# Kernel tuning notes

Hardware: AMD Instinct MI355X
Metric: run time of the kernel (lower is better)

Reference implementation:

```python
import jax, jax.numpy as jnp
import numpy as np

N_NODES = 200000
N_EDGES = 600000
IN_DIM = 130   # hidden_dim + 2
HID = 128
BN_EPS = 1e-5


def setup_inputs() -> dict:
    key = jax.random.key(0)
    ks = jax.random.split(key, 12)
    s = 0.05
    inp = {
        'x': jax.random.normal(ks[0], (N_NODES, IN_DIM), dtype=jnp.float32),
        'edge_index': jax.random.randint(ks[1], (2, N_EDGES), 0, N_NODES, dtype=jnp.int32),
        # SAGEConv 1: lin_l (aggregated neighbors, with bias), lin_r (root, no bias)
        'W1_l': jax.random.normal(ks[2], (IN_DIM, HID), dtype=jnp.float32) * s,
        'b1_l': jnp.zeros((HID,), dtype=jnp.float32),
        'W1_r': jax.random.normal(ks[3], (IN_DIM, HID), dtype=jnp.float32) * s,
        # BatchNorm1d(128) params + running stats (eval mode)
        'g1': jnp.ones((HID,), dtype=jnp.float32),
        'be1': jnp.zeros((HID,), dtype=jnp.float32),
        'rm1': jax.random.normal(ks[4], (HID,), dtype=jnp.float32) * 0.01,
        'rv1': jnp.ones((HID,), dtype=jnp.float32),
        # SAGEConv 2
        'W2_l': jax.random.normal(ks[5], (HID, HID), dtype=jnp.float32) * s,
        'b2_l': jnp.zeros((HID,), dtype=jnp.float32),
        'W2_r': jax.random.normal(ks[6], (HID, HID), dtype=jnp.float32) * s,
        'g2': jnp.ones((HID,), dtype=jnp.float32),
        'be2': jnp.zeros((HID,), dtype=jnp.float32),
        'rm2': jax.random.normal(ks[7], (HID,), dtype=jnp.float32) * 0.01,
        'rv2': jnp.ones((HID,), dtype=jnp.float32),
    }
    return inp


def _sage_mean(x, src, dst, W_l, b_l, W_r, n_nodes):
    # PyG SAGEConv (mean aggr): out = lin_l(mean_{j in N(i)} x_j) + lin_r(x_i)
    msg = x[src]                                                 # [E, F] gather
    agg = jax.ops.segment_sum(msg, dst, num_segments=n_nodes)    # [N, F]
    deg = jax.ops.segment_sum(jnp.ones((src.shape[0], 1), x.dtype), dst,
                              num_segments=n_nodes)              # [N, 1]
    mean = agg / jnp.maximum(deg, 1.0)
    return mean @ W_l + b_l + x @ W_r


def _bn_eval(x, g, b, rm, rv):
    return (x - rm) * (g * jax.lax.rsqrt(rv + BN_EPS)) + b


def reference(x, edge_index, W1_l, b1_l, W1_r, g1, be1, rm1, rv1,
              W2_l, b2_l, W2_r, g2, be2, rm2, rv2):
    src, dst = edge_index[0], edge_index[1]
    n = x.shape[0]
    h = _sage_mean(x, src, dst, W1_l, b1_l, W1_r, n)
    h = jax.nn.relu(_bn_eval(h, g1, be1, rm1, rv1))
    # dropout is identity in eval mode
    h = _sage_mean(h, src, dst, W2_l, b2_l, W2_r, n)
    h = jax.nn.relu(_bn_eval(h, g2, be2, rm2, rv2))
    return h
```

## Files before the change

### kernel.cpp

```cpp
#include <hip/hip_runtime.h>
#include <hip/hip_bf16.h>

typedef short v8s __attribute__((ext_vector_type(8)));
typedef float v4f __attribute__((ext_vector_type(4)));
typedef unsigned short v4us __attribute__((ext_vector_type(4)));

__device__ __forceinline__ unsigned short f2bf(float x) {
  union { float f; unsigned int u; } c; c.f = x;
  unsigned int u = c.u;
  return (unsigned short)((u + 0x7fffu + ((u >> 16) & 1u)) >> 16);
}
__device__ __forceinline__ float bflo(unsigned int u) {
  union { unsigned int u; float f; } c; c.u = u << 16; return c.f;
}
__device__ __forceinline__ float bfhi(unsigned int u) {
  union { unsigned int u; float f; } c; c.u = u & 0xffff0000u; return c.f;
}
__device__ __forceinline__ ushort2 pk(float2 v) {
  union { __hip_bfloat162 b; ushort2 u; } c;
  c.b = __float22bfloat162_rn(v);
  return c.u;
}
__device__ __forceinline__ v4us pk4(v4f v) {
  const ushort2 lo = pk(make_float2(v[0], v[1]));
  const ushort2 hi = pk(make_float2(v[2], v[3]));
  v4us r; r[0] = lo.x; r[1] = lo.y; r[2] = hi.x; r[3] = hi.y;
  return r;
}

__device__ __forceinline__ void pack2_dev(const float* __restrict__ Wl,
                                          const float* __restrict__ Wr,
                                          unsigned short* __restrict__ wpk,
                                          int K, int tot, int i) {
  if (i >= tot) return;
  const int kk = i & 31, n = (i >> 5) & 255, kc = i >> 13;
  const int k = kc * 32 + kk;
  float v = 0.f;
  if (k < K) v = (n < 128) ? Wl[k * 128 + n] : Wr[k * 128 + (n - 128)];
  wpk[i] = f2bf(v);
}

__global__ void setup_k(const float* __restrict__ g1, const float* __restrict__ be1,
                        const float* __restrict__ rm1, const float* __restrict__ rv1,
                        const float* __restrict__ b1,
                        const float* __restrict__ g2, const float* __restrict__ be2,
                        const float* __restrict__ rm2, const float* __restrict__ rv2,
                        const float* __restrict__ b2,
                        const float* __restrict__ W1l, const float* __restrict__ W1r,
                        const float* __restrict__ W2l, const float* __restrict__ W2r,
                        float* __restrict__ s1, float* __restrict__ t1,
                        float* __restrict__ s2, float* __restrict__ t2,
                        unsigned short* __restrict__ wp1, unsigned short* __restrict__ wp2,
                        unsigned short* __restrict__ bufA, int* __restrict__ degi,
                        int N, int NZB) {
  const int b = blockIdx.x, tid = threadIdx.x;
  if (b < NZB) {
    const int i = b * 256 + tid;
    if (i < N) degi[i] = 0;
    return;
  }
  int r = b - NZB;
  if (r < 160) { pack2_dev(W1l, W1r, wp1, 130, 5 * 8192, r * 256 + tid); return; }
  r -= 160;
  if (r < 128) { pack2_dev(W2l, W2r, wp2, 128, 4 * 8192, r * 256 + tid); return; }
  if (tid < 128) {
    float sv = g1[tid] * rsqrtf(rv1[tid] + 1e-5f);
    s1[tid] = sv; t1[tid] = (b1[tid] - rm1[tid]) * sv + be1[tid];
    float sw = g2[tid] * rsqrtf(rv2[tid] + 1e-5f);
    s2[tid] = sw; t2[tid] = (b2[tid] - rm2[tid]) * sw + be2[tid];
  }
  if (tid < 64) ((unsigned int*)(bufA + (long)N * 128))[tid] = 0u;
}

__global__ __launch_bounds__(256) void scan1_k(const int* __restrict__ degi,
                                               int* __restrict__ rowptr,
                                               int* __restrict__ bsum, int N) {
  __shared__ int sd[256];
  const int t = threadIdx.x;
  const int base = blockIdx.x * 1024 + t * 4;
  int v[4];
#pragma unroll
  for (int j = 0; j < 4; ++j) v[j] = (base + j < N) ? degi[base + j] : 0;
  const int tot = v[0] + v[1] + v[2] + v[3];
  sd[t] = tot;
  __syncthreads();
  for (int off = 1; off < 256; off <<= 1) {
    int o = (t >= off) ? sd[t - off] : 0;
    __syncthreads();
    sd[t] += o;
    __syncthreads();
  }
  int e = sd[t] - tot;
#pragma unroll
  for (int j = 0; j < 4; ++j) {
    if (base + j < N) rowptr[base + j] = e;
    e += v[j];
  }
  if (t == 255) bsum[blockIdx.x] = sd[255];
}
__global__ __launch_bounds__(256) void scan3_k(int* __restrict__ rowptr,
                                               int* __restrict__ cursor,
                                               const int* __restrict__ bsum,
                                               int N, int E) {
  __shared__ int sd[256];
  const int t = threadIdx.x;
  const int chunk = blockIdx.x >> 2;
  sd[t] = (t < chunk) ? bsum[t] : 0;
  __syncthreads();
  for (int off = 128; off >= 1; off >>= 1) {
    if (t < off) sd[t] += sd[t + off];
    __syncthreads();
  }
  const int S = sd[0];
  const int i = blockIdx.x * 256 + t;
  if (i < N) {
    const int v = rowptr[i] + S;
    rowptr[i] = v;
    cursor[i] = v;
  } else if (i == N) {
    rowptr[N] = E;
  }
}
__global__ void fill_k(const int* __restrict__ src, const int* __restrict__ dst,
                       int* __restrict__ cursor, int* __restrict__ nbr, int E) {
  int i = blockIdx.x * 256 + threadIdx.x;
  if (i < E) {
    int p = atomicAdd(&cursor[dst[i]], 1);
    nbr[p] = src[i];
  }
}

__global__ __launch_bounds__(256) void gemmc_k(const float* __restrict__ Asrc,
                                               const unsigned short* __restrict__ wpk,
                                               unsigned short* __restrict__ Ol,
                                               unsigned short* __restrict__ Or,
                                               const int* __restrict__ dst,
                                               int* __restrict__ degi,
                                               int N, int E, int ngb) {
  constexpr int KC = 5;
  constexpr int KP = KC * 32;
  constexpr int LDA = KP + 8;
  __shared__ __align__(16) unsigned short a_s[64][LDA];
  const int tid = threadIdx.x;

  if ((int)blockIdx.x >= ngb) {
    const int i = ((int)blockIdx.x - ngb) * 256 + tid;
    if (i < E) atomicAdd(&degi[dst[i]], 1);
    return;
  }

  const int node0 = blockIdx.x * 64;
  {
    const int zr = tid >> 2, zq = tid & 3;
    v8s z = {0, 0, 0, 0, 0, 0, 0, 0};
    *(v8s*)&a_s[zr][136 + zq * 8] = z;
    if (tid < 192) {
      const int r3 = tid / 3, p3 = tid - 3 * r3;
      *(unsigned int*)&a_s[r3][130 + 2 * p3] = 0u;
    }
  }
  const float* xb = Asrc + (long)node0 * 130;
  if (node0 + 64 <= N) {
    float4 v[9];
#pragma unroll
    for (int i = 0; i < 9; ++i) {
      const int g = i * 256 + tid;
      if (g < 2080) v[i] = *(const float4*)(xb + 4 * g);
    }
#pragma unroll
    for (int i = 0; i < 9; ++i) {
      const int g = i * 256 + tid;
      if (g < 2080) {
        const int p0 = 2 * g, p1 = 2 * g + 1;
        const int r0_ = (p0 * 4033) >> 18, r1_ = (p1 * 4033) >> 18;
        const int c0_ = p0 - 65 * r0_, c1_ = p1 - 65 * r1_;
        *(ushort2*)&a_s[r0_][2 * c0_] = pk(make_float2(v[i].x, v[i].y));
        *(ushort2*)&a_s[r1_][2 * c1_] = pk(make_float2(v[i].z, v[i].w));
      }
    }
  } else {
    for (int i = 0; i < 9; ++i) {
      const int g = i * 256 + tid;
      if (g < 2080) {
#pragma unroll
        for (int h = 0; h < 2; ++h) {
          const int p = 2 * g + h;
          const int r = (p * 4033) >> 18;
          const int c = p - 65 * r;
          float2 vv = make_float2(0.f, 0.f);
          if (node0 + r < N)
            vv = *(const float2*)(Asrc + (long)(node0 + r) * 130 + 2 * c);
          *(ushort2*)&a_s[r][2 * c] = pk(vv);
        }
      }
    }
  }
  __syncthreads();

  const int wave = tid >> 6, lane = tid & 63;
  const int quad = lane >> 4, l16 = lane & 15;
  v4f acc[4][4];
#pragma unroll
  for (int mt = 0; mt < 4; ++mt)
#pragma unroll
    for (int nt = 0; nt < 4; ++nt) acc[mt][nt] = (v4f){0.f, 0.f, 0.f, 0.f};

  const unsigned short* wb = wpk + (wave * 64 + l16) * 32 + quad * 8;
#pragma unroll
  for (int kc = 0; kc < KC; ++kc) {
    v8s wf[4];
#pragma unroll
    for (int nt = 0; nt < 4; ++nt)
      wf[nt] = *(const v8s*)(wb + kc * 8192 + nt * 512);
#pragma unroll
    for (int mt = 0; mt < 4; ++mt) {
      v8s nf = *(const v8s*)(&a_s[mt * 16 + l16][kc * 32 + quad * 8]);
#pragma unroll
      for (int nt = 0; nt < 4; ++nt)
        acc[mt][nt] = __builtin_amdgcn_mfma_f32_16x16x32_bf16(wf[nt], nf, acc[mt][nt], 0, 0, 0);
    }
  }

  unsigned short* ob = (wave < 2) ? Ol : Or;
  const int cb = (wave & 1) * 64;
#pragma unroll
  for (int mt = 0; mt < 4; ++mt) {
    const int rw = node0 + mt * 16 + l16;
    if (rw < N) {
#pragma unroll
      for (int nt = 0; nt < 4; ++nt)
        *(v4us*)(ob + (long)rw * 128 + cb + nt * 16 + quad * 4) = pk4(acc[mt][nt]);
    }
  }
}

__global__ __launch_bounds__(256) void gemmB_k(const unsigned short* __restrict__ Asrc,
                                               const unsigned short* __restrict__ wpk,
                                               unsigned short* __restrict__ Ol,
                                               unsigned short* __restrict__ Or, int N) {
  constexpr int KC = 4;
  constexpr int KP = KC * 32;
  constexpr int LDA = KP + 8;
  __shared__ __align__(16) unsigned short a_s[64][LDA];
  const int tid = threadIdx.x;
  const int node0 = blockIdx.x * 64;

  const unsigned short* hb = Asrc + (long)node0 * 128;
  v8s v[KC];
#pragma unroll
  for (int i = 0; i < KC; ++i) {
    const int u = i * 256 + tid;
    const int r = u >> 4;
    v[i] = (v8s){0, 0, 0, 0, 0, 0, 0, 0};
    if (node0 + r < N) v[i] = *(const v8s*)(hb + 8 * u);
  }
#pragma unroll
  for (int i = 0; i < KC; ++i) {
    const int u = i * 256 + tid;
    *(v8s*)&a_s[u >> 4][(u & 15) * 8] = v[i];
  }
  __syncthreads();

  const int wave = tid >> 6, lane = tid & 63;
  const int quad = lane >> 4, l16 = lane & 15;
  v4f acc[4][4];
#pragma unroll
  for (int mt = 0; mt < 4; ++mt)
#pragma unroll
    for (int nt = 0; nt < 4; ++nt) acc[mt][nt] = (v4f){0.f, 0.f, 0.f, 0.f};

  const unsigned short* wb = wpk + (wave * 64 + l16) * 32 + quad * 8;
#pragma unroll
  for (int kc = 0; kc < KC; ++kc) {
    v8s wf[4];
#pragma unroll
    for (int nt = 0; nt < 4; ++nt)
      wf[nt] = *(const v8s*)(wb + kc * 8192 + nt * 512);
#pragma unroll
    for (int mt = 0; mt < 4; ++mt) {
      v8s nf = *(const v8s*)(&a_s[mt * 16 + l16][kc * 32 + quad * 8]);
#pragma unroll
      for (int nt = 0; nt < 4; ++nt)
        acc[mt][nt] = __builtin_amdgcn_mfma_f32_16x16x32_bf16(wf[nt], nf, acc[mt][nt], 0, 0, 0);
    }
  }

  unsigned short* ob = (wave < 2) ? Ol : Or;
  const int cb = (wave & 1) * 64;
#pragma unroll
  for (int mt = 0; mt < 4; ++mt) {
    const int rw = node0 + mt * 16 + l16;
    if (rw < N) {
#pragma unroll
      for (int nt = 0; nt < 4; ++nt)
        *(v4us*)(ob + (long)rw * 128 + cb + nt * 16 + quad * 4) = pk4(acc[mt][nt]);
    }
  }
}

template<bool OUTF32>
__global__ __launch_bounds__(256) void spmmL_k(const unsigned short* __restrict__ gsrc,
                                               const unsigned short* __restrict__ rsrc,
                                               const int* __restrict__ rowptr,
                                               const int* __restrict__ nbr,
                                               const float* __restrict__ sc,
                                               const float* __restrict__ tc,
                                               void* __restrict__ out, int N, int E) {
  const int tid = threadIdx.x;
  const int lane = tid & 63;
  const int wu = __builtin_amdgcn_readfirstlane(tid >> 6);
  const int nb = blockIdx.x * 32 + wu * 8;

  int r0[8], d[8];
#pragma unroll
  for (int r = 0; r < 8; ++r) {
    const int i0 = min(nb + r, N);
    const int i1 = min(nb + r + 1, N);
    r0[r] = rowptr[i0];
    d[r] = (nb + r < N) ? (rowptr[i1] - r0[r]) : 0;
  }
  int dm = 0;
#pragma unroll
  for (int r = 0; r < 8; ++r) dm = max(dm, d[r]);

  float2 a[8];
#pragma unroll
  for (int r = 0; r < 8; ++r) a[r] = make_float2(0.f, 0.f);

  const int lofs = lane << 1;
  for (int e0 = 0; e0 < dm; e0 += 4) {
    unsigned int u[8][4];
#pragma unroll
    for (int r = 0; r < 8; ++r) {
      if (e0 < d[r]) {
#pragma unroll
        for (int j = 0; j < 4; ++j) {
          const int e = e0 + j;
          const int nv = nbr[min(r0[r] + e, E - 1)];
          const int idx = (e < d[r]) ? nv : N;
          u[r][j] = *(const unsigned int*)(gsrc + ((long)idx << 7) + lofs);
        }
      }
    }
#pragma unroll
    for (int r = 0; r < 8; ++r) {
      if (e0 < d[r]) {
#pragma unroll
        for (int j = 0; j < 4; ++j) {
          a[r].x += bflo(u[r][j]);
          a[r].y += bfhi(u[r][j]);
        }
      }
    }
  }

  const float2 sv = *(const float2*)(sc + lofs);
  const float2 tv = *(const float2*)(tc + lofs);
#pragma unroll
  for (int r = 0; r < 8; ++r) {
    if (nb + r < N) {
      const float inv = 1.0f / fmaxf((float)d[r], 1.0f);
      const unsigned int ur = *(const unsigned int*)(rsrc + ((long)(nb + r) << 7) + lofs);
      float yx = fmaxf((a[r].x * inv + bflo(ur)) * sv.x + tv.x, 0.f);
      float yy = fmaxf((a[r].y * inv + bfhi(ur)) * sv.y + tv.y, 0.f);
      if (OUTF32) {
        *(float2*)((float*)out + (long)(nb + r) * 128 + lofs) = make_float2(yx, yy);
      } else {
        *(ushort2*)((unsigned short*)out + (long)(nb + r) * 128 + lofs) =
            pk(make_float2(yx, yy));
      }
    }
  }
}

extern "C" void kernel_launch(void* const* d_in, const int* in_sizes, int n_in,
                              void* d_out, int out_size, void* d_ws, size_t ws_size,
                              hipStream_t stream) {
  const float* x   = (const float*)d_in[0];
  const int*   ei  = (const int*)d_in[1];
  const float* W1l = (const float*)d_in[2];
  const float* b1  = (const float*)d_in[3];
  const float* W1r = (const float*)d_in[4];
  const float* g1  = (const float*)d_in[5];
  const float* be1 = (const float*)d_in[6];
  const float* rm1 = (const float*)d_in[7];
  const float* rv1 = (const float*)d_in[8];
  const float* W2l = (const float*)d_in[9];
  const float* b2  = (const float*)d_in[10];
  const float* W2r = (const float*)d_in[11];
  const float* g2  = (const float*)d_in[12];
  const float* be2 = (const float*)d_in[13];
  const float* rm2 = (const float*)d_in[14];
  const float* rv2 = (const float*)d_in[15];

  const int E = in_sizes[1] / 2;
  const int N = in_sizes[0] / 130;
  const int* src = ei;
  const int* dst = ei + E;

  unsigned short* bufA = (unsigned short*)d_ws;
  unsigned short* bufB = bufA + (size_t)(N + 1) * 128;
  unsigned short* bufC = bufB + (size_t)(N + 1) * 128;
  unsigned short* wp1  = bufC + (size_t)N * 128;
  unsigned short* wp2  = wp1 + 5 * 8192;
  float* s1 = (float*)(wp2 + 4 * 8192);
  float* t1 = s1 + 128;
  float* s2 = t1 + 128;
  float* t2 = s2 + 128;
  int* degi   = (int*)(t2 + 128);
  int* rowptr = degi + N;
  int* bsum   = rowptr + N + 1;
  int* nbr    = bsum + 256;

  const int NZB = (N + 255) / 256;
  const int ngb = (N + 63) / 64;
  const int ecb = (E + 255) / 256;
  const int nsb = (N + 31) / 32;
  const int nb1k = (N + 1023) / 1024;

  hipLaunchKernelGGL(setup_k, dim3(NZB + 288 + 1), dim3(256), 0, stream,
                     g1, be1, rm1, rv1, b1, g2, be2, rm2, rv2, b2,
                     W1l, W1r, W2l, W2r, s1, t1, s2, t2,
                     wp1, wp2, bufA, degi, N, NZB);

  hipLaunchKernelGGL(gemmc_k, dim3(ngb + ecb), dim3(256), 0, stream,
                     x, wp1, bufA, bufB, dst, degi, N, E, ngb);

  hipLaunchKernelGGL(scan1_k, dim3(nb1k), dim3(256), 0, stream, degi, rowptr, bsum, N);
  hipLaunchKernelGGL(scan3_k, dim3((N + 256) / 256), dim3(256), 0, stream,
                     rowptr, degi, bsum, N, E);
  hipLaunchKernelGGL(fill_k, dim3(ecb), dim3(256), 0, stream,
                     src, dst, degi, nbr, E);

  hipLaunchKernelGGL((spmmL_k<false>), dim3(nsb), dim3(256), 0, stream,
                     bufA, bufB, rowptr, nbr, s1, t1, (void*)bufB, N, E);
  hipLaunchKernelGGL(gemmB_k, dim3(ngb), dim3(256), 0, stream,
                     bufB, wp2, bufA, bufC, N);
  hipLaunchKernelGGL((spmmL_k<true>), dim3(nsb), dim3(256), 0, stream,
                     bufA, bufC, rowptr, nbr, s2, t2, d_out, N, E);
}
```

Baseline: 419.5 us.

## Process two node tiles per GEMM block, prefetching the second tile during the first MFMA

```diff
diff --git a/kernel.cpp b/kernel.cpp
--- a/kernel.cpp
+++ b/kernel.cpp
@@ -1,5 +1,4 @@
 #include <hip/hip_runtime.h>
-#include <hip/hip_bf16.h>
 
 typedef short v8s __attribute__((ext_vector_type(8)));
 typedef float v4f __attribute__((ext_vector_type(4)));
@@ -17,14 +16,10 @@
   union { unsigned int u; float f; } c; c.u = u & 0xffff0000u; return c.f;
 }
 __device__ __forceinline__ ushort2 pk(float2 v) {
-  union { __hip_bfloat162 b; ushort2 u; } c;
-  c.b = __float22bfloat162_rn(v);
-  return c.u;
+  ushort2 p; p.x = f2bf(v.x); p.y = f2bf(v.y); return p;
 }
 __device__ __forceinline__ v4us pk4(v4f v) {
-  const ushort2 lo = pk(make_float2(v[0], v[1]));
-  const ushort2 hi = pk(make_float2(v[2], v[3]));
-  v4us r; r[0] = lo.x; r[1] = lo.y; r[2] = hi.x; r[3] = hi.y;
+  v4us r; r[0] = f2bf(v[0]); r[1] = f2bf(v[1]); r[2] = f2bf(v[2]); r[3] = f2bf(v[3]);
   return r;
 }
 
@@ -136,20 +131,25 @@
                                                unsigned short* __restrict__ Or,
                                                const int* __restrict__ dst,
                                                int* __restrict__ degi,
-                                               int N, int E, int ngb) {
+                                               int N, int E, int ng2, int T) {
   constexpr int KC = 5;
-  constexpr int KP = KC * 32;
-  constexpr int LDA = KP + 8;
-  __shared__ __align__(16) unsigned short a_s[64][LDA];
+  __shared__ __align__(16) unsigned short a_s[64][168];
   const int tid = threadIdx.x;
 
-  if ((int)blockIdx.x >= ngb) {
-    const int i = ((int)blockIdx.x - ngb) * 256 + tid;
+  if ((int)blockIdx.x >= ng2) {
+    const int i = ((int)blockIdx.x - ng2) * 256 + tid;
     if (i < E) atomicAdd(&degi[dst[i]], 1);
     return;
   }
 
-  const int node0 = blockIdx.x * 64;
+  const int t0 = blockIdx.x * 2;
+  const int t1 = t0 + 1;
+  const int wave = tid >> 6, lane = tid & 63;
+  const int quad = lane >> 4, l16 = lane & 15;
+  unsigned short* ob = (wave < 2) ? Ol : Or;
+  const int cb = (wave & 1) * 64;
+  const unsigned short* wb = wpk + (wave * 64 + l16) * 32 + quad * 8;
+
   {
     const int zr = tid >> 2, zq = tid & 3;
     v8s z = {0, 0, 0, 0, 0, 0, 0, 0};
@@ -159,9 +159,12 @@
       *(unsigned int*)&a_s[r3][130 + 2 * p3] = 0u;
     }
   }
-  const float* xb = Asrc + (long)node0 * 130;
-  if (node0 + 64 <= N) {
-    float4 v[9];
+
+  float4 v[9];
+  const int node00 = t0 * 64;
+  const bool full0 = (node00 + 64 <= N);
+  if (full0) {
+    const float* xb = Asrc + (long)node00 * 130;
 #pragma unroll
     for (int i = 0; i < 9; ++i) {
       const int g = i * 256 + tid;
@@ -188,8 +191,8 @@
           const int r = (p * 4033) >> 18;
           const int c = p - 65 * r;
           float2 vv = make_float2(0.f, 0.f);
-          if (node0 + r < N)
-            vv = *(const float2*)(Asrc + (long)(node0 + r) * 130 + 2 * c);
+          if (node00 + r < N)
+            vv = *(const float2*)(Asrc + (long)(node00 + r) * 130 + 2 * c);
           *(ushort2*)&a_s[r][2 * c] = pk(vv);
         }
       }
@@ -197,39 +200,110 @@
   }
   __syncthreads();
 
-  const int wave = tid >> 6, lane = tid & 63;
-  const int quad = lane >> 4, l16 = lane & 15;
-  v4f acc[4][4];
-#pragma unroll
-  for (int mt = 0; mt < 4; ++mt)
-#pragma unroll
-    for (int nt = 0; nt < 4; ++nt) acc[mt][nt] = (v4f){0.f, 0.f, 0.f, 0.f};
-
-  const unsigned short* wb = wpk + (wave * 64 + l16) * 32 + quad * 8;
-#pragma unroll
-  for (int kc = 0; kc < KC; ++kc) {
-    v8s wf[4];
-#pragma unroll
-    for (int nt = 0; nt < 4; ++nt)
-      wf[nt] = *(const v8s*)(wb + kc * 8192 + nt * 512);
+  const int node01 = t1 * 64;
+  const bool have1 = (t1 < T);
+  const bool full1 = have1 && (node01 + 64 <= N);
+  if (full1) {
+    const float* xb = Asrc + (long)node01 * 130;
+#pragma unroll
+    for (int i = 0; i < 9; ++i) {
+      const int g = i * 256 + tid;
+      if (g < 2080) v[i] = *(const float4*)(xb + 4 * g);
+    }
+  }
+
+  {
+    v4f acc[4][4];
+#pragma unroll
+    for (int mt = 0; mt < 4; ++mt)
+#pragma unroll
+      for (int nt = 0; nt < 4; ++nt) acc[mt][nt] = (v4f){0.f, 0.f, 0.f, 0.f};
+#pragma unroll
+    for (int kc = 0; kc < KC; ++kc) {
+      v8s wf[4];
+#pragma unroll
+      for (int nt = 0; nt < 4; ++nt)
+        wf[nt] = *(const v8s*)(wb + kc * 8192 + nt * 512);
+#pragma unroll
+      for (int mt = 0; mt < 4; ++mt) {
+        v8s nf = *(const v8s*)(&a_s[mt * 16 + l16][kc * 32 + quad * 8]);
+#pragma unroll
+        for (int nt = 0; nt < 4; ++nt)
+          acc[mt][nt] = __builtin_amdgcn_mfma_f32_16x16x32_bf16(wf[nt], nf, acc[mt][nt], 0, 0, 0);
+      }
+    }
 #pragma unroll
     for (int mt = 0; mt < 4; ++mt) {
-      v8s nf = *(const v8s*)(&a_s[mt * 16 + l16][kc * 32 + quad * 8]);
+      const int rw = node00 + mt * 16 + l16;
+      if (rw < N) {
+#pragma unroll
+        for (int nt = 0; nt < 4; ++nt)
+          *(v4us*)(ob + (long)rw * 128 + cb + nt * 16 + quad * 4) = pk4(acc[mt][nt]);
+      }
+    }
+  }
+  if (!have1) return;
+  __syncthreads();
+
+  if (full1) {
+#pragma unroll
+    for (int i = 0; i < 9; ++i) {
+      const int g = i * 256 + tid;
+      if (g < 2080) {
+        const int p0 = 2 * g, p1 = 2 * g + 1;
+        const int r0_ = (p0 * 4033) >> 18, r1_ = (p1 * 4033) >> 18;
+        const int c0_ = p0 - 65 * r0_, c1_ = p1 - 65 * r1_;
+        *(ushort2*)&a_s[r0_][2 * c0_] = pk(make_float2(v[i].x, v[i].y));
+        *(ushort2*)&a_s[r1_][2 * c1_] = pk(make_float2(v[i].z, v[i].w));
+      }
+    }
+  } else {
+    for (int i = 0; i < 9; ++i) {
+      const int g = i * 256 + tid;
+      if (g < 2080) {
+#pragma unroll
+        for (int h = 0; h < 2; ++h) {
+          const int p = 2 * g + h;
+          const int r = (p * 4033) >> 18;
+          const int c = p - 65 * r;
+          float2 vv = make_float2(0.f, 0.f);
+          if (node01 + r < N)
+            vv = *(const float2*)(Asrc + (long)(node01 + r) * 130 + 2 * c);
+          *(ushort2*)&a_s[r][2 * c] = pk(vv);
+        }
+      }
+    }
+  }
+  __syncthreads();
+
+  {
+    v4f acc[4][4];
+#pragma unroll
+    for (int mt = 0; mt < 4; ++mt)
+#pragma unroll
+      for (int nt = 0; nt < 4; ++nt) acc[mt][nt] = (v4f){0.f, 0.f, 0.f, 0.f};
+#pragma unroll
+    for (int kc = 0; kc < KC; ++kc) {
+      v8s wf[4];
 #pragma unroll
       for (int nt = 0; nt < 4; ++nt)
-        acc[mt][nt] = __builtin_amdgcn_mfma_f32_16x16x32_bf16(wf[nt], nf, acc[mt][nt], 0, 0, 0);
-    }
-  }
-
-  unsigned short* ob = (wave < 2) ? Ol : Or;
-  const int cb = (wave & 1) * 64;
-#pragma unroll
-  for (int mt = 0; mt < 4; ++mt) {
-    const int rw = node0 + mt * 16 + l16;
-    if (rw < N) {
-#pragma unroll
-      for (int nt = 0; nt < 4; ++nt)
-        *(v4us*)(ob + (long)rw * 128 + cb + nt * 16 + quad * 4) = pk4(acc[mt][nt]);
+        wf[nt] = *(const v8s*)(wb + kc * 8192 + nt * 512);
+#pragma unroll
+      for (int mt = 0; mt < 4; ++mt) {
+        v8s nf = *(const v8s*)(&a_s[mt * 16 + l16][kc * 32 + quad * 8]);
+#pragma unroll
+        for (int nt = 0; nt < 4; ++nt)
+          acc[mt][nt] = __builtin_amdgcn_mfma_f32_16x16x32_bf16(wf[nt], nf, acc[mt][nt], 0, 0, 0);
+      }
+    }
+#pragma unroll
+    for (int mt = 0; mt < 4; ++mt) {
+      const int rw = node01 + mt * 16 + l16;
+      if (rw < N) {
+#pragma unroll
+        for (int nt = 0; nt < 4; ++nt)
+          *(v4us*)(ob + (long)rw * 128 + cb + nt * 16 + quad * 4) = pk4(acc[mt][nt]);
+      }
     }
   }
 }
@@ -237,63 +311,121 @@
 __global__ __launch_bounds__(256) void gemmB_k(const unsigned short* __restrict__ Asrc,
                                                const unsigned short* __restrict__ wpk,
                                                unsigned short* __restrict__ Ol,
-                                               unsigned short* __restrict__ Or, int N) {
+                                               unsigned short* __restrict__ Or,
+                                               int N, int T) {
   constexpr int KC = 4;
-  constexpr int KP = KC * 32;
-  constexpr int LDA = KP + 8;
-  __shared__ __align__(16) unsigned short a_s[64][LDA];
+  __shared__ __align__(16) unsigned short a_s[64][136];
   const int tid = threadIdx.x;
-  const int node0 = blockIdx.x * 64;
-
-  const unsigned short* hb = Asrc + (long)node0 * 128;
-  v8s v[KC];
-#pragma unroll
-  for (int i = 0; i < KC; ++i) {
-    const int u = i * 256 + tid;
-    const int r = u >> 4;
-    v[i] = (v8s){0, 0, 0, 0, 0, 0, 0, 0};
-    if (node0 + r < N) v[i] = *(const v8s*)(hb + 8 * u);
-  }
-#pragma unroll
-  for (int i = 0; i < KC; ++i) {
-    const int u = i * 256 + tid;
-    *(v8s*)&a_s[u >> 4][(u & 15) * 8] = v[i];
-  }
-  __syncthreads();
-
+  const int t0 = blockIdx.x * 2;
+  const int t1 = t0 + 1;
   const int wave = tid >> 6, lane = tid & 63;
   const int quad = lane >> 4, l16 = lane & 15;
-  v4f acc[4][4];
-#pragma unroll
-  for (int mt = 0; mt < 4; ++mt)
-#pragma unroll
-    for (int nt = 0; nt < 4; ++nt) acc[mt][nt] = (v4f){0.f, 0.f, 0.f, 0.f};
-
-  const unsigned short* wb = wpk + (wave * 64 + l16) * 32 + quad * 8;
-#pragma unroll
-  for (int kc = 0; kc < KC; ++kc) {
-    v8s wf[4];
-#pragma unroll
-    for (int nt = 0; nt < 4; ++nt)
-      wf[nt] = *(const v8s*)(wb + kc * 8192 + nt * 512);
-#pragma unroll
-    for (int mt = 0; mt < 4; ++mt) {
-      v8s nf = *(const v8s*)(&a_s[mt * 16 + l16][kc * 32 + quad * 8]);
-#pragma unroll
-      for (int nt = 0; nt < 4; ++nt)
-        acc[mt][nt] = __builtin_amdgcn_mfma_f32_16x16x32_bf16(wf[nt], nf, acc[mt][nt], 0, 0, 0);
-    }
-  }
-
   unsigned short* ob = (wave < 2) ? Ol : Or;
   const int cb = (wave & 1) * 64;
-#pragma unroll
-  for (int mt = 0; mt < 4; ++mt) {
-    const int rw = node0 + mt * 16 + l16;
-    if (rw < N) {
+  const unsigned short* wb = wpk + (wave * 64 + l16) * 32 + quad * 8;
+
+  v8s v[KC];
+  const int node00 = t0 * 64;
+  {
+    const unsigned short* hb = Asrc + (long)node00 * 128;
+#pragma unroll
+    for (int i = 0; i < KC; ++i) {
+      const int u = i * 256 + tid;
+      const int r = u >> 4;
+      v[i] = (v8s){0, 0, 0, 0, 0, 0, 0, 0};
+      if (node00 + r < N) v[i] = *(const v8s*)(hb + 8 * u);
+    }
+#pragma unroll
+    for (int i = 0; i < KC; ++i) {
+      const int u = i * 256 + tid;
+      *(v8s*)&a_s[u >> 4][(u & 15) * 8] = v[i];
+    }
+  }
+  __syncthreads();
+
+  const int node01 = t1 * 64;
+  const bool have1 = (t1 < T);
+  if (have1) {
+    const unsigned short* hb = Asrc + (long)node01 * 128;
+#pragma unroll
+    for (int i = 0; i < KC; ++i) {
+      const int u = i * 256 + tid;
+      const int r = u >> 4;
+      v[i] = (v8s){0, 0, 0, 0, 0, 0, 0, 0};
+      if (node01 + r < N) v[i] = *(const v8s*)(hb + 8 * u);
+    }
+  }
+
+  {
+    v4f acc[4][4];
+#pragma unroll
+    for (int mt = 0; mt < 4; ++mt)
+#pragma unroll
+      for (int nt = 0; nt < 4; ++nt) acc[mt][nt] = (v4f){0.f, 0.f, 0.f, 0.f};
+#pragma unroll
+    for (int kc = 0; kc < KC; ++kc) {
+      v8s wf[4];
 #pragma unroll
       for (int nt = 0; nt < 4; ++nt)
-        *(v4us*)(ob + (long)rw * 128 + cb + nt * 16 + quad * 4) = pk4(acc[mt][nt]);
+        wf[nt] = *(const v8s*)(wb + kc * 8192 + nt * 512);
+#pragma unroll
+      for (int mt = 0; mt < 4; ++mt) {
+        v8s nf = *(const v8s*)(&a_s[mt * 16 + l16][kc * 32 + quad * 8]);
+#pragma unroll
+        for (int nt = 0; nt < 4; ++nt)
+          acc[mt][nt] = __builtin_amdgcn_mfma_f32_16x16x32_bf16(wf[nt], nf, acc[mt][nt], 0, 0, 0);
+      }
+    }
+#pragma unroll
+    for (int mt = 0; mt < 4; ++mt) {
+      const int rw = node00 + mt * 16 + l16;
+      if (rw < N) {
+#pragma unroll
+        for (int nt = 0; nt < 4; ++nt)
+          *(v4us*)(ob + (long)rw * 128 + cb + nt * 16 + quad * 4) = pk4(acc[mt][nt]);
+      }
+    }
+  }
+  if (!have1) return;
+  __syncthreads();
+
+  {
+#pragma unroll
+    for (int i = 0; i < KC; ++i) {
+      const int u = i * 256 + tid;
+      *(v8s*)&a_s[u >> 4][(u & 15) * 8] = v[i];
+    }
+  }
+  __syncthreads();
+
+  {
+    v4f acc[4][4];
+#pragma unroll
+    for (int mt = 0; mt < 4; ++mt)
+#pragma unroll
+      for (int nt = 0; nt < 4; ++nt) acc[mt][nt] = (v4f){0.f, 0.f, 0.f, 0.f};
+#pragma unroll
+    for (int kc = 0; kc < KC; ++kc) {
+      v8s wf[4];
+#pragma unroll
+      for (int nt = 0; nt < 4; ++nt)
+        wf[nt] = *(const v8s*)(wb + kc * 8192 + nt * 512);
+#pragma unroll
+      for (int mt = 0; mt < 4; ++mt) {
+        v8s nf = *(const v8s*)(&a_s[mt * 16 + l16][kc * 32 + quad * 8]);
+#pragma unroll
+        for (int nt = 0; nt < 4; ++nt)
+          acc[mt][nt] = __builtin_amdgcn_mfma_f32_16x16x32_bf16(wf[nt], nf, acc[mt][nt], 0, 0, 0);
+      }
+    }
+#pragma unroll
+    for (int mt = 0; mt < 4; ++mt) {
+      const int rw = node01 + mt * 16 + l16;
+      if (rw < N) {
+#pragma unroll
+        for (int nt = 0; nt < 4; ++nt)
+          *(v4us*)(ob + (long)rw * 128 + cb + nt * 16 + quad * 4) = pk4(acc[mt][nt]);
+      }
     }
   }
 }
@@ -413,7 +545,8 @@
   int* nbr    = bsum + 256;
 
   const int NZB = (N + 255) / 256;
-  const int ngb = (N + 63) / 64;
+  const int T   = (N + 63) / 64;
+  const int ng2 = (T + 1) / 2;
   const int ecb = (E + 255) / 256;
   const int nsb = (N + 31) / 32;
   const int nb1k = (N + 1023) / 1024;
@@ -423,8 +556,8 @@
                      W1l, W1r, W2l, W2r, s1, t1, s2, t2,
                      wp1, wp2, bufA, degi, N, NZB);
 
-  hipLaunchKernelGGL(gemmc_k, dim3(ngb + ecb), dim3(256), 0, stream,
-                     x, wp1, bufA, bufB, dst, degi, N, E, ngb);
+  hipLaunchKernelGGL(gemmc_k, dim3(ng2 + ecb), dim3(256), 0, stream,
+                     x, wp1, bufA, bufB, dst, degi, N, E, ng2, T);
 
   hipLaunchKernelGGL(scan1_k, dim3(nb1k), dim3(256), 0, stream, degi, rowptr, bsum, N);
   hipLaunchKernelGGL(scan3_k, dim3((N + 256) / 256), dim3(256), 0, stream,
@@ -434,8 +567,8 @@
 
   hipLaunchKernelGGL((spmmL_k<false>), dim3(nsb), dim3(256), 0, stream,
                      bufA, bufB, rowptr, nbr, s1, t1, (void*)bufB, N, E);
-  hipLaunchKernelGGL(gemmB_k, dim3(ngb), dim3(256), 0, stream,
-                     bufB, wp2, bufA, bufC, N);
+  hipLaunchKernelGGL(gemmB_k, dim3(ng2), dim3(256), 0, stream,
+                     bufB, wp2, bufA, bufC, N, T);
   hipLaunchKernelGGL((spmmL_k<true>), dim3(nsb), dim3(256), 0, stream,
                      bufA, bufC, rowptr, nbr, s2, t2, d_out, N, E);
 }
```

After: 422.9 us. No clear change (+0.8%).
